# Kernel optimization log

Measured on AMD Instinct MI355X. Metric: run time of the kernel, lower is better.

Reference implementation:

```python
import jax, jax.numpy as jnp
import numpy as np

B, T, C, H, L, V = 4, 1024, 1024, 16, 6, 32000
D = C // H
STD = 0.02


def setup_inputs() -> dict:
    key = jax.random.key(0)
    ks = jax.random.split(key, 12)
    return {
        "idx": jax.random.randint(ks[0], (B, T), 0, V),
        "tok_emb": jax.random.normal(ks[1], (V, C), jnp.float32) * STD,
        "pos_emb": jax.random.normal(ks[2], (T, C), jnp.float32) * STD,
        "qkv_w": jax.random.normal(ks[3], (L, C, 3 * C), jnp.float32) * STD,
        "attn_out_w": jax.random.normal(ks[4], (L, C, C), jnp.float32) * STD,
        "attn_out_b": jnp.zeros((L, C), jnp.float32),
        "fc1_w": jax.random.normal(ks[5], (L, C, 4 * C), jnp.float32) * STD,
        "fc1_b": jnp.zeros((L, 4 * C), jnp.float32),
        "fc2_w": jax.random.normal(ks[6], (L, 4 * C, C), jnp.float32) * STD,
        "fc2_b": jnp.zeros((L, C), jnp.float32),
        "ln1_w": jnp.ones((L, C), jnp.float32),
        "ln1_b": jnp.zeros((L, C), jnp.float32),
        "ln2_w": jnp.ones((L, C), jnp.float32),
        "ln2_b": jnp.zeros((L, C), jnp.float32),
        "lnf_w": jnp.ones((C,), jnp.float32),
        "lnf_b": jnp.zeros((C,), jnp.float32),
        "head_w": jax.random.normal(ks[7], (C, V), jnp.float32) * STD,
    }


def layernorm(x, w, b, eps=1e-5):
    mu = jnp.mean(x, axis=-1, keepdims=True)
    var = jnp.var(x, axis=-1, keepdims=True)
    return (x - mu) * jax.lax.rsqrt(var + eps) * w + b


def attention(x, qkv_w, out_w, out_b, causal_mask):
    # x: (B,T,C)
    qkv = jnp.einsum("btc,cf->btf", x, qkv_w)  # (B,T,3C)
    q, k, v = jnp.split(qkv, 3, axis=-1)
    q = q.reshape(B, T, H, D).transpose(0, 2, 1, 3)  # (B,H,T,D)
    k = k.reshape(B, T, H, D).transpose(0, 2, 1, 3)
    v = v.reshape(B, T, H, D).transpose(0, 2, 1, 3)
    scores = jnp.einsum("bhqd,bhkd->bhqk", q, k) / np.sqrt(D).astype(np.float32)
    scores = jnp.where(causal_mask, scores, -jnp.inf)
    w = jax.nn.softmax(scores, axis=-1)
    out = jnp.einsum("bhqk,bhkd->bhqd", w, v)  # (B,H,T,D)
    out = out.transpose(0, 2, 1, 3).reshape(B, T, C)
    return jnp.einsum("btc,cd->btd", out, out_w) + out_b


def reference(idx, tok_emb, pos_emb, qkv_w, attn_out_w, attn_out_b,
              fc1_w, fc1_b, fc2_w, fc2_b, ln1_w, ln1_b, ln2_w, ln2_b,
              lnf_w, lnf_b, head_w):
    causal_mask = jnp.tril(jnp.ones((T, T), dtype=bool))[None, None]  # (1,1,T,T)
    x = tok_emb[idx] + pos_emb[jnp.arange(T)][None]  # (B,T,C)
    for l in range(L):
        h = layernorm(x, ln1_w[l], ln1_b[l])
        x = x + attention(h, qkv_w[l], attn_out_w[l], attn_out_b[l], causal_mask)
        h = layernorm(x, ln2_w[l], ln2_b[l])
        h = jax.nn.relu(jnp.einsum("btc,cf->btf", h, fc1_w[l]) + fc1_b[l])
        x = x + jnp.einsum("btf,fc->btc", h, fc2_w[l]) + fc2_b[l]
    x = layernorm(x, lnf_w, lnf_b)
    logits = jnp.einsum("btc,cv->btv", x, head_w)  # (B,T,V)
    return logits
```

## Files before the change

kernel.cpp:

```cpp
#include <hip/hip_runtime.h>
#include <cstdint>
#include <cstddef>

typedef __bf16 bf16_t;
typedef __bf16 bf16x8 __attribute__((ext_vector_type(8)));
typedef float f32x4 __attribute__((ext_vector_type(4)));
typedef int i32x4 __attribute__((ext_vector_type(4)));

#define B_ 4
#define T_ 1024
#define C_ 1024
#define H_ 16
#define L_ 6
#define V_ 32000
#define M_ (B_ * T_)

__global__ __launch_bounds__(256) void k_embed(const int* __restrict__ idx,
                                               const float* __restrict__ tok,
                                               const float* __restrict__ pos,
                                               float* __restrict__ x) {
  int row = blockIdx.x;
  int t = row & (T_ - 1);
  int id = idx[row];
  int c = threadIdx.x * 4;
  f32x4 a = *(const f32x4*)(tok + (size_t)id * C_ + c);
  f32x4 p = *(const f32x4*)(pos + (size_t)t * C_ + c);
  *(f32x4*)(x + (size_t)row * C_ + c) = a + p;
}

__global__ __launch_bounds__(256) void k_ln(const float* __restrict__ x,
                                            const float* __restrict__ w,
                                            const float* __restrict__ b,
                                            bf16_t* __restrict__ out) {
  __shared__ float red[8];
  int row = blockIdx.x;
  int tid = threadIdx.x;
  const float* xr = x + (size_t)row * C_;
  f32x4 v = *(const f32x4*)(xr + tid * 4);
  float s = v[0] + v[1] + v[2] + v[3];
  float q = v[0] * v[0] + v[1] * v[1] + v[2] * v[2] + v[3] * v[3];
#pragma unroll
  for (int off = 32; off; off >>= 1) {
    s += __shfl_xor(s, off);
    q += __shfl_xor(q, off);
  }
  int wid = tid >> 6;
  if ((tid & 63) == 0) { red[wid * 2] = s; red[wid * 2 + 1] = q; }
  __syncthreads();
  s = red[0] + red[2] + red[4] + red[6];
  q = red[1] + red[3] + red[5] + red[7];
  float mu = s * (1.f / C_);
  float var = q * (1.f / C_) - mu * mu;
  float rstd = rsqrtf(var + 1e-5f);
  f32x4 wv = *(const f32x4*)(w + tid * 4);
  f32x4 bv = *(const f32x4*)(b + tid * 4);
  bf16_t* o = out + (size_t)row * C_ + tid * 4;
#pragma unroll
  for (int j = 0; j < 4; j++) o[j] = (bf16_t)((v[j] - mu) * rstd * wv[j] + bv[j]);
}

__global__ __launch_bounds__(256) void k_transpose_bf16(const float* __restrict__ in,
                                                        bf16_t* __restrict__ out,
                                                        int K, int N) {
  __shared__ float tile[32][33];
  int n0 = blockIdx.x * 32, k0 = blockIdx.y * 32;
  int tid = threadIdx.x;
  int cr = tid >> 5, cc = tid & 31;
#pragma unroll
  for (int it = 0; it < 4; it++) {
    int r = it * 8 + cr;
    tile[r][cc] = in[(size_t)(k0 + r) * N + n0 + cc];
  }
  __syncthreads();
#pragma unroll
  for (int it = 0; it < 4; it++) {
    int r = it * 8 + cr;
    out[(size_t)(n0 + r) * K + k0 + cc] = (bf16_t)tile[cc][r];
  }
}

__global__ __launch_bounds__(256) void k_reshape_qk(const bf16_t* __restrict__ qkv,
                                                    bf16_t* __restrict__ qh,
                                                    bf16_t* __restrict__ kh) {
  int g = blockIdx.x * 256 + threadIdx.x;
  int d = g & 63;
  int t = (g >> 6) & (T_ - 1);
  int h = (g >> 16) & (H_ - 1);
  int b = g >> 20;
  size_t src = ((size_t)(b * T_ + t)) * (3 * C_) + h * 64 + d;
  qh[g] = (bf16_t)((float)qkv[src] * 0.125f);
  kh[g] = qkv[src + C_];
}

__global__ __launch_bounds__(256) void k_vtrans(const bf16_t* __restrict__ qkv,
                                                bf16_t* __restrict__ vT) {
  __shared__ bf16_t tile[64][65];
  int bh = blockIdx.x;
  int t0 = blockIdx.y * 64;
  int tid = threadIdx.x;
  int c = tid & 63, rr = tid >> 6;
  int b = bh >> 4, h = bh & (H_ - 1);
  const bf16_t* src = qkv + ((size_t)(b * T_ + t0)) * (3 * C_) + 2 * C_ + h * 64;
#pragma unroll
  for (int it = 0; it < 16; it++) {
    int r = it * 4 + rr;
    tile[r][c] = src[(size_t)r * (3 * C_) + c];
  }
  __syncthreads();
  bf16_t* dst = vT + (size_t)bh * 64 * T_ + t0;
#pragma unroll
  for (int it = 0; it < 16; it++) {
    int dr = it * 4 + rr;
    dst[(size_t)dr * T_ + c] = tile[c][dr];
  }
}

__global__ __launch_bounds__(256) void k_attn(const bf16_t* __restrict__ qh,
                                              const bf16_t* __restrict__ kh,
                                              const bf16_t* __restrict__ vT,
                                              bf16_t* __restrict__ outb) {
  __shared__ bf16_t p_lds[4][16 * 32];
  int tid = threadIdx.x, lane = tid & 63, wid = tid >> 6;
  int bh = blockIdx.x;
  int b = bh >> 4, h = bh & (H_ - 1);
  int qbase = blockIdx.y * 64 + wid * 16;
  const bf16_t* qp = qh + ((size_t)bh * T_ + qbase) * 64;
  const bf16_t* kp = kh + (size_t)bh * T_ * 64;
  const bf16_t* vp = vT + (size_t)bh * 64 * T_;
  int r = lane & 15, g = lane >> 4;

  bf16x8 qf0 = *(const bf16x8*)(qp + r * 64 + g * 8);
  bf16x8 qf1 = *(const bf16x8*)(qp + r * 64 + 32 + g * 8);

  f32x4 o[4];
  float m[4], l[4];
#pragma unroll
  for (int j = 0; j < 4; j++) { m[j] = -1e30f; l[j] = 0.f; o[j] = (f32x4){0.f, 0.f, 0.f, 0.f}; }

  int kv_end = qbase + 16;
  for (int jb = 0; jb < kv_end; jb += 32) {
    f32x4 s0 = (f32x4){0.f, 0.f, 0.f, 0.f};
    f32x4 s1 = (f32x4){0.f, 0.f, 0.f, 0.f};
    const bf16_t* kb0 = kp + (size_t)(jb + r) * 64 + g * 8;
    const bf16_t* kb1 = kb0 + 16 * 64;
    s0 = __builtin_amdgcn_mfma_f32_16x16x32_bf16(qf0, *(const bf16x8*)(kb0), s0, 0, 0, 0);
    s0 = __builtin_amdgcn_mfma_f32_16x16x32_bf16(qf1, *(const bf16x8*)(kb0 + 32), s0, 0, 0, 0);
    s1 = __builtin_amdgcn_mfma_f32_16x16x32_bf16(qf0, *(const bf16x8*)(kb1), s1, 0, 0, 0);
    s1 = __builtin_amdgcn_mfma_f32_16x16x32_bf16(qf1, *(const bf16x8*)(kb1 + 32), s1, 0, 0, 0);

    float p0[4], p1[4], fac[4];
#pragma unroll
    for (int j = 0; j < 4; j++) {
      int rowg = qbase + g * 4 + j;
      float v0 = s0[j], v1 = s1[j];
      if (jb + r > rowg) v0 = -1e30f;
      if (jb + 16 + r > rowg) v1 = -1e30f;
      float t = fmaxf(v0, v1);
      t = fmaxf(t, __shfl_xor(t, 1));
      t = fmaxf(t, __shfl_xor(t, 2));
      t = fmaxf(t, __shfl_xor(t, 4));
      t = fmaxf(t, __shfl_xor(t, 8));
      float nm = fmaxf(m[j], t);
      p0[j] = __expf(v0 - nm);
      p1[j] = __expf(v1 - nm);
      float f = __expf(m[j] - nm);
      float ts = p0[j] + p1[j];
      ts += __shfl_xor(ts, 1);
      ts += __shfl_xor(ts, 2);
      ts += __shfl_xor(ts, 4);
      ts += __shfl_xor(ts, 8);
      l[j] = l[j] * f + ts;
      m[j] = nm;
      fac[j] = f;
    }
    f32x4 fv = (f32x4){fac[0], fac[1], fac[2], fac[3]};
#pragma unroll
    for (int d = 0; d < 4; d++) o[d] *= fv;

    bf16_t* pl = p_lds[wid];
#pragma unroll
    for (int j = 0; j < 4; j++) {
      pl[(g * 4 + j) * 32 + r] = (bf16_t)p0[j];
      pl[(g * 4 + j) * 32 + 16 + r] = (bf16_t)p1[j];
    }
    bf16x8 pa = *(const bf16x8*)(pl + r * 32 + g * 8);
#pragma unroll
    for (int d = 0; d < 4; d++) {
      const bf16_t* vf = vp + (size_t)(d * 16 + r) * T_ + jb + g * 8;
      o[d] = __builtin_amdgcn_mfma_f32_16x16x32_bf16(pa, *(const bf16x8*)(vf), o[d], 0, 0, 0);
    }
  }

#pragma unroll
  for (int d = 0; d < 4; d++) {
#pragma unroll
    for (int j = 0; j < 4; j++) {
      float val = o[d][j] / l[j];
      outb[((size_t)(b * T_ + qbase + g * 4 + j)) * C_ + h * 64 + d * 16 + r] = (bf16_t)val;
    }
  }
}

__device__ __forceinline__ void gld_lds16(const bf16_t* g, bf16_t* l) {
  __builtin_amdgcn_global_load_lds((const __attribute__((address_space(1))) void*)g,
                                   (__attribute__((address_space(3))) void*)l, 16, 0, 0);
}
__device__ __forceinline__ bf16x8 lds_rd128(uint32_t addr) {
  i32x4 d;
  asm volatile("ds_read_b128 %0, %1" : "=v"(d) : "v"(addr));
  return __builtin_bit_cast(bf16x8, d);
}
#define BAR_() __builtin_amdgcn_s_barrier()
#define SCHED0_() __builtin_amdgcn_sched_barrier(0)
#define WLGN_(n)                                                           \
  do {                                                                     \
    asm volatile("s_waitcnt lgkmcnt(" #n ")" ::: "memory");                \
    SCHED0_();                                                             \
  } while (0)

template <int OUTBF, int HASB, int HASRELU, int HASRES>
__global__ __launch_bounds__(256, 2) void k_gemm(const bf16_t* __restrict__ A,
                                                 const bf16_t* __restrict__ Bt,
                                                 const float* __restrict__ bias,
                                                 const float* resid,
                                                 void* Cout, int M, int N, int K) {
  __shared__ bf16_t As[2][128][64];
  __shared__ bf16_t Bs[2][128][64];
  bf16_t* AsF = &As[0][0][0];
  bf16_t* BsF = &Bs[0][0][0];
  const uint32_t asb = (uint32_t)(uintptr_t)AsF;
  const uint32_t bsb = (uint32_t)(uintptr_t)BsF;

  int tid = threadIdx.x, lane = tid & 63, w = tid >> 6;
  int wr = w >> 1, wc = w & 1;
  int r15 = lane & 15, g4 = lane >> 4;

  int nwg = (int)(gridDim.x * gridDim.y);
  int bid = (int)(blockIdx.y * gridDim.x + blockIdx.x);
  int xcd = bid & 7, loc = bid >> 3;
  int q8 = nwg >> 3, r8 = nwg & 7;
  int swz = (xcd < r8) ? xcd * (q8 + 1) + loc : r8 * (q8 + 1) + (xcd - r8) * q8 + loc;
  int nY = M >> 7;
  int by = swz % nY, bx = swz / nY;
  size_t rowBase = (size_t)by * 128;
  size_t colBase = (size_t)bx * 128;

  int srowL = (lane >> 3);
  int scol = ((lane & 7) ^ srowL) * 8;

  uint32_t xm = (uint32_t)((r15 & 7) << 4);
  uint32_t offK0 = ((uint32_t)(g4 * 16)) ^ xm;
  uint32_t offK1 = ((uint32_t)(g4 * 16 + 64)) ^ xm;
  uint32_t aRd = asb + (uint32_t)((wr * 64 + r15) * 128);
  uint32_t bRd = bsb + (uint32_t)((wc * 64 + r15) * 128);

  f32x4 acc[4][4];
#pragma unroll
  for (int i = 0; i < 4; i++)
#pragma unroll
    for (int j = 0; j < 4; j++) acc[i][j] = (f32x4){0.f, 0.f, 0.f, 0.f};

  bf16x8 a0[4], a1[4], b0[4], b1[4];

#define KSTAGE_(tk, bufv)                                                            \
  do {                                                                               \
    _Pragma("unroll") for (int _q = 0; _q < 4; _q++) {                               \
      int _row = _q * 32 + w * 8 + srowL;                                            \
      const bf16_t* _ga = A + (rowBase + _row) * (size_t)K + (size_t)(tk)*64 + scol; \
      const bf16_t* _gb = Bt + (colBase + _row) * (size_t)K + (size_t)(tk)*64 + scol;\
      gld_lds16(_ga, AsF + (bufv)*8192 + _q * 2048 + w * 512);                       \
      gld_lds16(_gb, BsF + (bufv)*8192 + _q * 2048 + w * 512);                       \
    }                                                                                \
  } while (0)

#define KRDS_(aset, bset, kk, bufv)                                                  \
  do {                                                                               \
    uint32_t _off = (kk) ? offK1 : offK0;                                            \
    uint32_t _ab = aRd + (uint32_t)(bufv)*16384u + _off;                             \
    uint32_t _bb = bRd + (uint32_t)(bufv)*16384u + _off;                             \
    _Pragma("unroll") for (int _m = 0; _m < 4; _m++)                                 \
        aset[_m] = lds_rd128(_ab + _m * 2048);                                       \
    _Pragma("unroll") for (int _n = 0; _n < 4; _n++)                                 \
        bset[_n] = lds_rd128(_bb + _n * 2048);                                       \
  } while (0)

#define KMFH_(aset, bset)                                                            \
  do {                                                                               \
    __builtin_amdgcn_s_setprio(1);                                                   \
    _Pragma("unroll") for (int _m = 0; _m < 4; _m++)                                 \
        _Pragma("unroll") for (int _n = 0; _n < 4; _n++)                             \
            acc[_m][_n] = __builtin_amdgcn_mfma_f32_16x16x32_bf16(                   \
                aset[_m], bset[_n], acc[_m][_n], 0, 0, 0);                           \
    __builtin_amdgcn_s_setprio(0);                                                   \
  } while (0)

  KSTAGE_(0, 0);
  asm volatile("s_waitcnt vmcnt(0)" ::: "memory");
  BAR_();

  int NT = K >> 6;
  for (int kt = 0; kt < NT; ++kt) {
    int buf = kt & 1;
    bool pf = (kt + 1 < NT);
    if (pf) KSTAGE_(kt + 1, buf ^ 1);
    KRDS_(a0, b0, 0, buf);
    KRDS_(a1, b1, 1, buf);
    WLGN_(8);
    KMFH_(a0, b0);
    WLGN_(0);
    KMFH_(a1, b1);
    asm volatile("s_waitcnt vmcnt(0)" ::: "memory");
    BAR_();
  }

#pragma unroll
  for (int i = 0; i < 4; i++) {
    size_t row0 = rowBase + wr * 64 + i * 16 + g4 * 4;
#pragma unroll
    for (int j = 0; j < 4; j++) {
      size_t col = colBase + wc * 64 + j * 16 + r15;
      float bi = HASB ? bias[col] : 0.f;
#pragma unroll
      for (int q = 0; q < 4; q++) {
        size_t row = row0 + q;
        float v = acc[i][j][q] + bi;
        if (HASRELU) v = fmaxf(v, 0.f);
        if (HASRES) v += resid[row * (size_t)N + col];
        if (OUTBF)
          ((bf16_t*)Cout)[row * (size_t)N + col] = (bf16_t)v;
        else
          ((float*)Cout)[row * (size_t)N + col] = v;
      }
    }
  }
#undef KSTAGE_
#undef KRDS_
#undef KMFH_
}

#define STAGE_(q, tk, bufv)                                                           \
  do {                                                                                \
    const bf16_t* _ga = A + (size_t)(rowBase + (q)*64 + srow) * (size_t)K +           \
                        (size_t)(tk)*64 + scol;                                       \
    const bf16_t* _gb = Bt + (size_t)(colBase + (q)*64 + srow) * (size_t)K +          \
                        (size_t)(tk)*64 + scol;                                       \
    gld_lds16(_ga, AsF + (bufv)*16384 + (q)*4096 + w * 512);                          \
    gld_lds16(_gb, BsF + (bufv)*16384 + (q)*4096 + w * 512);                          \
  } while (0)

#define RDS_(aset, bset, kk, bufv)                                                    \
  do {                                                                                \
    uint32_t _off = (kk) ? offK1 : offK0;                                             \
    uint32_t _ab = aRd + (uint32_t)(bufv)*32768u + _off;                              \
    uint32_t _bb = bRd + (uint32_t)(bufv)*32768u + _off;                              \
    _Pragma("unroll") for (int _m = 0; _m < 8; _m++)                                  \
        aset[_m] = lds_rd128(_ab + _m * 2048);                                        \
    _Pragma("unroll") for (int _n = 0; _n < 4; _n++)                                  \
        bset[_n] = lds_rd128(_bb + _n * 2048);                                        \
  } while (0)

#define MFH_(aset, bset)                                                              \
  do {                                                                                \
    __builtin_amdgcn_s_setprio(1);                                                    \
    _Pragma("unroll") for (int _m = 0; _m < 8; _m++)                                  \
        _Pragma("unroll") for (int _n = 0; _n < 4; _n++)                              \
            acc[_m][_n] = __builtin_amdgcn_mfma_f32_16x16x32_bf16(                    \
                aset[_m], bset[_n], acc[_m][_n], 0, 0, 0);                            \
    __builtin_amdgcn_s_setprio(0);                                                    \
  } while (0)

template <int OUTBF, int HASB, int HASRELU, int HASRES>
__global__ __launch_bounds__(512, 2) void k_gemm256(const bf16_t* __restrict__ A,
                                                    const bf16_t* __restrict__ Bt,
                                                    const float* __restrict__ bias,
                                                    const float* resid,
                                                    void* Cout, int M, int N, int K) {
  __shared__ bf16_t As[2][256][64];
  __shared__ bf16_t Bs[2][256][64];
  bf16_t* AsF = &As[0][0][0];
  bf16_t* BsF = &Bs[0][0][0];
  const uint32_t asb = (uint32_t)(uintptr_t)AsF;
  const uint32_t bsb = (uint32_t)(uintptr_t)BsF;

  int tid = threadIdx.x, lane = tid & 63, w = tid >> 6;
  int wr = w >> 2, wc = w & 3;
  int r15 = lane & 15, g4 = lane >> 4;

  int nwg = (int)gridDim.x;
  int bid = (int)blockIdx.x;
  int xcd = bid & 7, loc = bid >> 3;
  int q8 = nwg >> 3, r8 = nwg & 7;
  int swz = (xcd < r8) ? xcd * (q8 + 1) + loc : r8 * (q8 + 1) + (xcd - r8) * q8 + loc;
  int nY = M >> 8;
  int by = swz % nY, bx = swz / nY;
  int rowBase = by * 256, colBase = bx * 256;

  int srow = w * 8 + (lane >> 3);
  int scol = ((lane & 7) ^ (lane >> 3)) * 8;

  uint32_t xm = (uint32_t)((r15 & 7) << 4);
  uint32_t offK0 = ((uint32_t)(g4 * 16)) ^ xm;
  uint32_t offK1 = ((uint32_t)(g4 * 16 + 64)) ^ xm;
  uint32_t aRd = asb + (uint32_t)((wr * 128 + r15) * 128);
  uint32_t bRd = bsb + (uint32_t)((wc * 64 + r15) * 128);

  f32x4 acc[8][4];
#pragma unroll
  for (int i = 0; i < 8; i++)
#pragma unroll
    for (int j = 0; j < 4; j++) acc[i][j] = (f32x4){0.f, 0.f, 0.f, 0.f};

  bf16x8 a0[8], a1[8], b0[4], b1[4];

#pragma unroll
  for (int q = 0; q < 4; q++) STAGE_(q, 0, 0);
  asm volatile("s_waitcnt vmcnt(0)" ::: "memory");
  BAR_();

  int NT = K >> 6;
  for (int kt = 0; kt < NT; ++kt) {
    int buf = kt & 1;
    bool pf = (kt + 1 < NT);
    if (pf) {
#pragma unroll
      for (int q = 0; q < 4; q++) STAGE_(q, kt + 1, buf ^ 1);
    }
    RDS_(a0, b0, 0, buf);
    RDS_(a1, b1, 1, buf);
    WLGN_(12);
    MFH_(a0, b0);
    WLGN_(0);
    MFH_(a1, b1);
    asm volatile("s_waitcnt vmcnt(0)" ::: "memory");
    BAR_();
  }

#pragma unroll
  for (int m = 0; m < 8; m++) {
    size_t row0 = (size_t)rowBase + wr * 128 + m * 16 + g4 * 4;
#pragma unroll
    for (int n = 0; n < 4; n++) {
      size_t col = (size_t)colBase + wc * 64 + n * 16 + r15;
      float bi = HASB ? bias[col] : 0.f;
#pragma unroll
      for (int qq = 0; qq < 4; qq++) {
        size_t row = row0 + qq;
        float v = acc[m][n][qq] + bi;
        if (HASRELU) v = fmaxf(v, 0.f);
        if (HASRES) v += resid[row * (size_t)N + col];
        if (OUTBF)
          ((bf16_t*)Cout)[row * (size_t)N + col] = (bf16_t)v;
        else
          ((float*)Cout)[row * (size_t)N + col] = v;
      }
    }
  }
}

extern "C" void kernel_launch(void* const* d_in, const int* in_sizes, int n_in,
                              void* d_out, int out_size, void* d_ws, size_t ws_size,
                              hipStream_t stream) {
  (void)in_sizes; (void)n_in; (void)out_size; (void)ws_size;
  const int* idx = (const int*)d_in[0];
  const float* tok_emb = (const float*)d_in[1];
  const float* pos_emb = (const float*)d_in[2];
  const float* qkv_w = (const float*)d_in[3];
  const float* attn_out_w = (const float*)d_in[4];
  const float* attn_out_b = (const float*)d_in[5];
  const float* fc1_w = (const float*)d_in[6];
  const float* fc1_b = (const float*)d_in[7];
  const float* fc2_w = (const float*)d_in[8];
  const float* fc2_b = (const float*)d_in[9];
  const float* ln1_w = (const float*)d_in[10];
  const float* ln1_b = (const float*)d_in[11];
  const float* ln2_w = (const float*)d_in[12];
  const float* ln2_b = (const float*)d_in[13];
  const float* lnf_w = (const float*)d_in[14];
  const float* lnf_b = (const float*)d_in[15];
  const float* head_w = (const float*)d_in[16];
  float* out = (float*)d_out;

  char* wsp = (char*)d_ws;
  auto alloc = [&](size_t bytes) {
    char* p = wsp;
    wsp += (bytes + 255) & ~(size_t)255;
    return p;
  };
  float* x      = (float*)alloc((size_t)M_ * C_ * 4);
  bf16_t* hbuf  = (bf16_t*)alloc((size_t)M_ * C_ * 2);
  bf16_t* qkvb  = (bf16_t*)alloc((size_t)M_ * 3 * C_ * 2);
  bf16_t* qhb   = (bf16_t*)alloc((size_t)M_ * C_ * 2);
  bf16_t* khb   = (bf16_t*)alloc((size_t)M_ * C_ * 2);
  bf16_t* vTb   = (bf16_t*)alloc((size_t)M_ * C_ * 2);
  bf16_t* attnb = (bf16_t*)alloc((size_t)M_ * C_ * 2);
  bf16_t* midb  = (bf16_t*)alloc((size_t)M_ * 4 * C_ * 2);
  bf16_t* qkvwT = (bf16_t*)alloc((size_t)3 * C_ * C_ * 2);
  bf16_t* owT   = (bf16_t*)alloc((size_t)C_ * C_ * 2);
  bf16_t* fc1wT = (bf16_t*)alloc((size_t)4 * C_ * C_ * 2);
  bf16_t* fc2wT = (bf16_t*)alloc((size_t)4 * C_ * C_ * 2);
  bf16_t* headwT= (bf16_t*)alloc((size_t)C_ * V_ * 2);

  k_embed<<<M_, 256, 0, stream>>>(idx, tok_emb, pos_emb, x);
  k_transpose_bf16<<<dim3(V_ / 32, C_ / 32), 256, 0, stream>>>(head_w, headwT, C_, V_);

  for (int l = 0; l < L_; l++) {
    k_transpose_bf16<<<dim3(3 * C_ / 32, C_ / 32), 256, 0, stream>>>(
        qkv_w + (size_t)l * C_ * 3 * C_, qkvwT, C_, 3 * C_);
    k_transpose_bf16<<<dim3(C_ / 32, C_ / 32), 256, 0, stream>>>(
        attn_out_w + (size_t)l * C_ * C_, owT, C_, C_);
    k_transpose_bf16<<<dim3(4 * C_ / 32, C_ / 32), 256, 0, stream>>>(
        fc1_w + (size_t)l * C_ * 4 * C_, fc1wT, C_, 4 * C_);
    k_transpose_bf16<<<dim3(C_ / 32, 4 * C_ / 32), 256, 0, stream>>>(
        fc2_w + (size_t)l * 4 * C_ * C_, fc2wT, 4 * C_, C_);

    k_ln<<<M_, 256, 0, stream>>>(x, ln1_w + l * C_, ln1_b + l * C_, hbuf);
    k_gemm<1, 0, 0, 0><<<dim3(3 * C_ / 128, M_ / 128), 256, 0, stream>>>(
        hbuf, qkvwT, nullptr, nullptr, qkvb, M_, 3 * C_, C_);
    k_reshape_qk<<<(M_ * C_) / 256, 256, 0, stream>>>(qkvb, qhb, khb);
    k_vtrans<<<dim3(B_ * H_, T_ / 64), 256, 0, stream>>>(qkvb, vTb);
    k_attn<<<dim3(B_ * H_, T_ / 64), 256, 0, stream>>>(qhb, khb, vTb, attnb);
    k_gemm<0, 1, 0, 1><<<dim3(C_ / 128, M_ / 128), 256, 0, stream>>>(
        attnb, owT, attn_out_b + l * C_, x, x, M_, C_, C_);

    k_ln<<<M_, 256, 0, stream>>>(x, ln2_w + l * C_, ln2_b + l * C_, hbuf);
    k_gemm<1, 1, 1, 0><<<dim3(4 * C_ / 128, M_ / 128), 256, 0, stream>>>(
        hbuf, fc1wT, fc1_b + (size_t)l * 4 * C_, nullptr, midb, M_, 4 * C_, C_);
    k_gemm<0, 1, 0, 1><<<dim3(C_ / 128, M_ / 128), 256, 0, stream>>>(
        midb, fc2wT, fc2_b + l * C_, x, x, M_, C_, 4 * C_);
  }

  k_ln<<<M_, 256, 0, stream>>>(x, lnf_w, lnf_b, hbuf);
  k_gemm256<0, 0, 0, 0><<<dim3((V_ / 256) * (M_ / 256)), 512, 0, stream>>>(
      hbuf, headwT, nullptr, nullptr, out, M_, V_, C_);
}
```

Measured before the change: 2.109 ms.

## Fuse QKV head-split into GEMM epilogue and batch per-layer weight transposes

The QKV GEMM epilogue now writes Q, K and V straight into head-major (B,H,T,D) buffers, which removes the separate reshape kernel and the extra round trip of the full qkv tensor through memory. The 1/sqrt(D) scale on Q is folded into the transposed weights during conversion. The four per-layer weight transpose launches are merged into one kernel, and vtrans now reads the contiguous V head buffer. The scattered epilogue stores may coalesce less well than the row-major writes did, and pre-scaling the weights changes where bf16 rounding happens.

```diff
diff --git a/kernel.cpp b/kernel.cpp
--- a/kernel.cpp
+++ b/kernel.cpp
@@ -79,32 +79,52 @@
   }
 }
 
-__global__ __launch_bounds__(256) void k_reshape_qk(const bf16_t* __restrict__ qkv,
-                                                    bf16_t* __restrict__ qh,
-                                                    bf16_t* __restrict__ kh) {
-  int g = blockIdx.x * 256 + threadIdx.x;
-  int d = g & 63;
-  int t = (g >> 6) & (T_ - 1);
-  int h = (g >> 16) & (H_ - 1);
-  int b = g >> 20;
-  size_t src = ((size_t)(b * T_ + t)) * (3 * C_) + h * 64 + d;
-  qh[g] = (bf16_t)((float)qkv[src] * 0.125f);
-  kh[g] = qkv[src + C_];
-}
-
-__global__ __launch_bounds__(256) void k_vtrans(const bf16_t* __restrict__ qkv,
+__global__ __launch_bounds__(256) void k_transpose_layer(
+    const float* __restrict__ qkvw, const float* __restrict__ attnw,
+    const float* __restrict__ fc1w, const float* __restrict__ fc2w,
+    bf16_t* __restrict__ qkvT, bf16_t* __restrict__ owT,
+    bf16_t* __restrict__ fc1T, bf16_t* __restrict__ fc2T) {
+  __shared__ float tile[32][33];
+  int tb = blockIdx.x;
+  const float* in;
+  bf16_t* out;
+  int K, N;
+  bool qs = false;
+  if (tb < 3072) { in = qkvw; out = qkvT; K = 1024; N = 3072; qs = true; }
+  else if (tb < 4096) { tb -= 3072; in = attnw; out = owT; K = 1024; N = 1024; }
+  else if (tb < 8192) { tb -= 4096; in = fc1w; out = fc1T; K = 1024; N = 4096; }
+  else { tb -= 8192; in = fc2w; out = fc2T; K = 4096; N = 1024; }
+  int nTx = N >> 5;
+  int n0 = (tb % nTx) * 32, k0 = (tb / nTx) * 32;
+  int tid = threadIdx.x;
+  int cr = tid >> 5, cc = tid & 31;
+#pragma unroll
+  for (int it = 0; it < 4; it++) {
+    int r = it * 8 + cr;
+    tile[r][cc] = in[(size_t)(k0 + r) * N + n0 + cc];
+  }
+  __syncthreads();
+#pragma unroll
+  for (int it = 0; it < 4; it++) {
+    int r = it * 8 + cr;
+    float v = tile[cc][r];
+    if (qs && (n0 + r) < 1024) v *= 0.125f;
+    out[(size_t)(n0 + r) * K + k0 + cc] = (bf16_t)v;
+  }
+}
+
+__global__ __launch_bounds__(256) void k_vtrans(const bf16_t* __restrict__ vh,
                                                 bf16_t* __restrict__ vT) {
   __shared__ bf16_t tile[64][65];
   int bh = blockIdx.x;
   int t0 = blockIdx.y * 64;
   int tid = threadIdx.x;
   int c = tid & 63, rr = tid >> 6;
-  int b = bh >> 4, h = bh & (H_ - 1);
-  const bf16_t* src = qkv + ((size_t)(b * T_ + t0)) * (3 * C_) + 2 * C_ + h * 64;
+  const bf16_t* src = vh + ((size_t)bh * T_ + t0) * 64;
 #pragma unroll
   for (int it = 0; it < 16; it++) {
     int r = it * 4 + rr;
-    tile[r][c] = src[(size_t)r * (3 * C_) + c];
+    tile[r][c] = src[(size_t)r * 64 + c];
   }
   __syncthreads();
   bf16_t* dst = vT + (size_t)bh * 64 * T_ + t0;
@@ -218,7 +238,7 @@
     SCHED0_();                                                             \
   } while (0)
 
-template <int OUTBF, int HASB, int HASRELU, int HASRES>
+template <int MODE, int HASB, int HASRELU, int HASRES>
 __global__ __launch_bounds__(256, 2) void k_gemm(const bf16_t* __restrict__ A,
                                                  const bf16_t* __restrict__ Bt,
                                                  const float* __restrict__ bias,
@@ -326,10 +346,18 @@
         float v = acc[i][j][q] + bi;
         if (HASRELU) v = fmaxf(v, 0.f);
         if (HASRES) v += resid[row * (size_t)N + col];
-        if (OUTBF)
+        if (MODE == 2) {
+          int part = (int)(col >> 10);
+          int within = (int)col & 1023;
+          int hh = within >> 6, dd = within & 63;
+          int bb = (int)(row >> 10), tt = (int)row & 1023;
+          bf16_t* dstp = (bf16_t*)Cout + (size_t)part * ((size_t)M_ * C_);
+          dstp[(((size_t)(bb * 16 + hh)) * 1024 + tt) * 64 + dd] = (bf16_t)v;
+        } else if (MODE == 1) {
           ((bf16_t*)Cout)[row * (size_t)N + col] = (bf16_t)v;
-        else
+        } else {
           ((float*)Cout)[row * (size_t)N + col] = v;
+        }
       }
     }
   }
@@ -488,9 +516,9 @@
   };
   float* x      = (float*)alloc((size_t)M_ * C_ * 4);
   bf16_t* hbuf  = (bf16_t*)alloc((size_t)M_ * C_ * 2);
-  bf16_t* qkvb  = (bf16_t*)alloc((size_t)M_ * 3 * C_ * 2);
-  bf16_t* qhb   = (bf16_t*)alloc((size_t)M_ * C_ * 2);
-  bf16_t* khb   = (bf16_t*)alloc((size_t)M_ * C_ * 2);
+  bf16_t* qhb   = (bf16_t*)alloc((size_t)3 * M_ * C_ * 2);
+  bf16_t* khb   = qhb + (size_t)M_ * C_;
+  bf16_t* vhb   = khb + (size_t)M_ * C_;
   bf16_t* vTb   = (bf16_t*)alloc((size_t)M_ * C_ * 2);
   bf16_t* attnb = (bf16_t*)alloc((size_t)M_ * C_ * 2);
   bf16_t* midb  = (bf16_t*)alloc((size_t)M_ * 4 * C_ * 2);
@@ -504,20 +532,15 @@
   k_transpose_bf16<<<dim3(V_ / 32, C_ / 32), 256, 0, stream>>>(head_w, headwT, C_, V_);
 
   for (int l = 0; l < L_; l++) {
-    k_transpose_bf16<<<dim3(3 * C_ / 32, C_ / 32), 256, 0, stream>>>(
-        qkv_w + (size_t)l * C_ * 3 * C_, qkvwT, C_, 3 * C_);
-    k_transpose_bf16<<<dim3(C_ / 32, C_ / 32), 256, 0, stream>>>(
-        attn_out_w + (size_t)l * C_ * C_, owT, C_, C_);
-    k_transpose_bf16<<<dim3(4 * C_ / 32, C_ / 32), 256, 0, stream>>>(
-        fc1_w + (size_t)l * C_ * 4 * C_, fc1wT, C_, 4 * C_);
-    k_transpose_bf16<<<dim3(C_ / 32, 4 * C_ / 32), 256, 0, stream>>>(
-        fc2_w + (size_t)l * 4 * C_ * C_, fc2wT, 4 * C_, C_);
+    k_transpose_layer<<<12288, 256, 0, stream>>>(
+        qkv_w + (size_t)l * C_ * 3 * C_, attn_out_w + (size_t)l * C_ * C_,
+        fc1_w + (size_t)l * C_ * 4 * C_, fc2_w + (size_t)l * 4 * C_ * C_,
+        qkvwT, owT, fc1wT, fc2wT);
 
     k_ln<<<M_, 256, 0, stream>>>(x, ln1_w + l * C_, ln1_b + l * C_, hbuf);
-    k_gemm<1, 0, 0, 0><<<dim3(3 * C_ / 128, M_ / 128), 256, 0, stream>>>(
-        hbuf, qkvwT, nullptr, nullptr, qkvb, M_, 3 * C_, C_);
-    k_reshape_qk<<<(M_ * C_) / 256, 256, 0, stream>>>(qkvb, qhb, khb);
-    k_vtrans<<<dim3(B_ * H_, T_ / 64), 256, 0, stream>>>(qkvb, vTb);
+    k_gemm<2, 0, 0, 0><<<dim3(3 * C_ / 128, M_ / 128), 256, 0, stream>>>(
+        hbuf, qkvwT, nullptr, nullptr, qhb, M_, 3 * C_, C_);
+    k_vtrans<<<dim3(B_ * H_, T_ / 64), 256, 0, stream>>>(vhb, vTb);
     k_attn<<<dim3(B_ * H_, T_ / 64), 256, 0, stream>>>(qhb, khb, vTb, attnb);
     k_gemm<0, 1, 0, 1><<<dim3(C_ / 128, M_ / 128), 256, 0, stream>>>(
         attnb, owT, attn_out_b + l * C_, x, x, M_, C_, C_);
```

New measurement: 2.056 ms. 2.5% less time.
